# Kernel tuning notes

Measured on AMD Instinct MI355X. Metric: run time of the kernel, lower is better.

Reference implementation:

```python
import jax, jax.numpy as jnp
import numpy as np

VOCAB = 30000
FEAT = 30000
HID = 1024
EMB = 1024
B, LQ, LKV = 32, 256, 256


def setup_inputs() -> dict:
    key = jax.random.key(0)
    ks = jax.random.split(key, 8)
    captions = jax.random.randint(ks[0], (B, LKV), 0, VOCAB)
    targets_feature = jax.random.randint(ks[1], (B, LKV), 0, FEAT)
    hidden_state = jax.random.normal(ks[2], (B, LQ, HID), dtype=jnp.float32)
    feature_mask = jax.random.uniform(ks[3], (B, LQ, LKV), dtype=jnp.float32)
    # embeddings initialized uniform(-0.1, 0.1) per init_weights
    Wa = jax.random.uniform(ks[4], (VOCAB, HID), minval=-0.1, maxval=0.1, dtype=jnp.float32)
    Wc = jax.random.uniform(ks[5], (FEAT, HID), minval=-0.1, maxval=0.1, dtype=jnp.float32)
    r = np.sqrt(6.0) / np.sqrt(2 * HID + EMB)
    fc_w = jax.random.uniform(ks[6], (EMB, 2 * HID), minval=-r, maxval=r, dtype=jnp.float32)
    fc_b = jnp.zeros((EMB,), dtype=jnp.float32)
    return {"captions": captions, "hidden_state": hidden_state,
            "targets_feature": targets_feature, "feature_mask": feature_mask,
            "Wa": Wa, "Wc": Wc, "fc_w": fc_w, "fc_b": fc_b}


def reference(captions, hidden_state, targets_feature, feature_mask, Wa, Wc, fc_w, fc_b):
    ea = Wa[captions]           # [B, LKV, H]
    ec = Wc[targets_feature]    # [B, LKV, H]
    # u = hidden_state @ embedding_a^T : [B, LQ, LKV]
    u = jnp.einsum('bqh,bkh->bqk', hidden_state, ea)
    mask = jnp.clip(feature_mask, 0.0, 1.0)
    delta = jnp.exp(u) * mask
    p = delta / (jnp.sum(delta, axis=2, keepdims=True) + 1e-10)  # masked softmax-like weights
    # weighted value sum without materializing [B,LQ,LKV,H] broadcasts
    o = jnp.einsum('bqk,bkh->bqh', p, ec)
    o = jnp.concatenate([hidden_state, o], axis=2)               # [B, LQ, 2H]
    o = o @ fc_w.T + fc_b                                        # [B, LQ, EMB]
    o = o + 1e-10
    norm = jnp.sqrt(jnp.sum(o * o, axis=-1, keepdims=True)) + 1e-8
    return o / norm
```

## Files before the change

### kernel.cpp

```cpp
#include <hip/hip_runtime.h>
#include <hip/hip_bf16.h>

typedef __attribute__((ext_vector_type(8))) short short8;
typedef __attribute__((ext_vector_type(4))) float f32x4;
using bf16 = __hip_bfloat16;


__device__ __forceinline__ void glds16(const void* g, void* lds) {
  __builtin_amdgcn_global_load_lds(
      (const __attribute__((address_space(1))) void*)g,
      (__attribute__((address_space(3))) void*)lds, 16, 0, 0);
}

__global__ __launch_bounds__(256) void k1_prep(
    const int* __restrict__ captions, const float* __restrict__ Wa,
    const float* __restrict__ H, const float* __restrict__ fcw,
    const int* __restrict__ targets, const float* __restrict__ Wc,
    bf16* __restrict__ EA, bf16* __restrict__ X, bf16* __restrict__ FW,
    bf16* __restrict__ ECT) {
  __shared__ float T[64][67];
  int task = blockIdx.x;
  int tid = threadIdx.x;
  if (task < 17408) {
    const float* src;
    bf16* dst;
    int n;
    if (task < 8192) {
      src = Wa + (size_t)captions[task] * 1024;
      dst = EA + (size_t)task * 1024;
      n = 1024;
    } else if (task < 16384) {
      int t = task - 8192;
      src = H + (size_t)t * 1024;
      dst = X + (size_t)t * 2048;
      n = 1024;
    } else {
      int t = task - 16384;
      src = fcw + (size_t)t * 2048;
      dst = FW + (size_t)t * 2048;
      n = 2048;
    }
    for (int c = tid * 4; c < n; c += 1024) {
      float4 v = *(const float4*)(src + c);
      __hip_bfloat162 p0, p1;
      p0.x = __float2bfloat16(v.x); p0.y = __float2bfloat16(v.y);
      p1.x = __float2bfloat16(v.z); p1.y = __float2bfloat16(v.w);
      *(__hip_bfloat162*)(dst + c) = p0;
      *(__hip_bfloat162*)(dst + c + 2) = p1;
    }
    return;
  }
  int bid = task - 17408;
  int b = bid >> 6;
  int kt = (bid >> 4) & 3;
  int ht = bid & 15;
#pragma unroll
  for (int p = 0; p < 4; ++p) {
    int k = p * 16 + (tid >> 4);
    int idx = targets[b * 256 + kt * 64 + k];
    const float* s = Wc + (size_t)idx * 1024 + ht * 64 + (tid & 15) * 4;
    float4 v = *(const float4*)s;
    int c = (tid & 15) * 4;
    T[k][c] = v.x; T[k][c + 1] = v.y; T[k][c + 2] = v.z; T[k][c + 3] = v.w;
  }
  __syncthreads();
#pragma unroll
  for (int p = 0; p < 8; ++p) {
    int h = p * 8 + (tid >> 5);
    int k = (tid & 31) * 2;
    __hip_bfloat162 o;
    o.x = __float2bfloat16(T[k][h]);
    o.y = __float2bfloat16(T[k + 1][h]);
    *(__hip_bfloat162*)(ECT + ((size_t)b * 1024 + ht * 64 + h) * 256 + kt * 64 + k) = o;
  }
}

__global__ __launch_bounds__(256, 1) void k23_scores_pv(
    bf16* __restrict__ X, const bf16* __restrict__ EA,
    const bf16* __restrict__ ECT, const float* __restrict__ mask) {
  __shared__ __align__(16) char smem[16 * 1024 + 512 + 128 * 1024];
  bf16* p_lds = (bf16*)smem;
  float* red  = (float*)(smem + 16 * 1024);
  bf16* big   = (bf16*)(smem + 16 * 1024 + 512);

  int p = blockIdx.x;
  int wg = (p & 7) * 32 + (p >> 3);
  int b = wg >> 3;
  int mb = wg & 7;
  int tid = threadIdx.x, w = tid >> 6, l = tid & 63;

  const bf16* Ag = X + ((size_t)b * 256 + mb * 32) * 2048;
  const bf16* Bg = EA + (size_t)b * 256 * 1024;
  bf16* As = big;
  bf16* Bs = big + 32 * 64;

  f32x4 sacc[2][4];
  f32x4 zero = {0.f, 0.f, 0.f, 0.f};
#pragma unroll
  for (int m2 = 0; m2 < 2; ++m2)
#pragma unroll
    for (int n = 0; n < 4; ++n) sacc[m2][n] = zero;

  for (int kt = 0; kt < 16; ++kt) {
    {
      int row = tid >> 3, ss = (tid & 7) ^ (row & 7);
      glds16(Ag + (size_t)row * 2048 + kt * 64 + ss * 8,
             As + (size_t)w * 64 * 8);
    }
#pragma unroll
    for (int i = 0; i < 8; ++i) {
      int c = i * 256 + tid;
      int row = c >> 3, ss = (c & 7) ^ (row & 7);
      glds16(Bg + (size_t)row * 1024 + kt * 64 + ss * 8,
             Bs + (size_t)(i * 256 + w * 64) * 8);
    }
    __syncthreads();
#pragma unroll
    for (int kk = 0; kk < 2; ++kk) {
      short8 a2[2];
#pragma unroll
      for (int m2 = 0; m2 < 2; ++m2) {
        int ar = m2 * 16 + (l & 15);
        int sl = kk * 4 + (l >> 4);
        a2[m2] = *(const short8*)(As + ar * 64 + ((sl ^ (ar & 7)) * 8));
      }
#pragma unroll
      for (int n = 0; n < 4; ++n) {
        int rb = w * 64 + n * 16 + (l & 15);
        int sl = kk * 4 + (l >> 4);
        short8 bfr = *(const short8*)(Bs + rb * 64 + ((sl ^ (rb & 7)) * 8));
#pragma unroll
        for (int m2 = 0; m2 < 2; ++m2)
          sacc[m2][n] = __builtin_amdgcn_mfma_f32_16x16x32_bf16(
              a2[m2], bfr, sacc[m2][n], 0, 0, 0);
      }
    }
    __syncthreads();
  }

  const float* mrow = mask + ((size_t)b * 256 + mb * 32) * 256;
  float s[2][4] = {{0.f, 0.f, 0.f, 0.f}, {0.f, 0.f, 0.f, 0.f}};
#pragma unroll
  for (int m2 = 0; m2 < 2; ++m2)
#pragma unroll
    for (int n = 0; n < 4; ++n)
#pragma unroll
      for (int i = 0; i < 4; ++i) {
        int r = m2 * 16 + ((l >> 4) << 2) + i;
        int c = w * 64 + n * 16 + (l & 15);
        float mv = mrow[r * 256 + c];
        mv = fminf(fmaxf(mv, 0.f), 1.f);
        float ev = expf(sacc[m2][n][i]) * mv;
        sacc[m2][n][i] = ev;
        s[m2][i] += ev;
      }
#pragma unroll
  for (int msk = 1; msk < 16; msk <<= 1)
#pragma unroll
    for (int m2 = 0; m2 < 2; ++m2)
#pragma unroll
      for (int i = 0; i < 4; ++i) s[m2][i] += __shfl_xor(s[m2][i], msk, 64);
  if ((l & 15) == 0) {
#pragma unroll
    for (int m2 = 0; m2 < 2; ++m2)
#pragma unroll
      for (int i = 0; i < 4; ++i)
        red[w * 32 + m2 * 16 + ((l >> 4) << 2) + i] = s[m2][i];
  }
  __syncthreads();
  float inv[2][4];
#pragma unroll
  for (int m2 = 0; m2 < 2; ++m2)
#pragma unroll
    for (int i = 0; i < 4; ++i) {
      int r = m2 * 16 + ((l >> 4) << 2) + i;
      float tot = red[r] + red[32 + r] + red[64 + r] + red[96 + r];
      inv[m2][i] = 1.f / (tot + 1e-10f);
    }
#pragma unroll
  for (int m2 = 0; m2 < 2; ++m2)
#pragma unroll
    for (int n = 0; n < 4; ++n)
#pragma unroll
      for (int i = 0; i < 4; ++i) {
        int r = m2 * 16 + ((l >> 4) << 2) + i;
        int c = w * 64 + n * 16 + (l & 15);
        float pv = sacc[m2][n][i] * inv[m2][i];
        p_lds[r * 256 + (((c >> 3) ^ (r & 7)) << 3) + (c & 7)] =
            __float2bfloat16(pv);
      }
  __syncthreads();

  bf16* XO = X + ((size_t)b * 256 + mb * 32) * 2048 + 1024;
  for (int np = 0; np < 2; ++np) {
    f32x4 acc[2][8];
#pragma unroll
    for (int m2 = 0; m2 < 2; ++m2)
#pragma unroll
      for (int n = 0; n < 8; ++n) acc[m2][n] = zero;

#pragma unroll
    for (int it = 0; it < 16; ++it) {
      int g = it * 64 + l;
      int row = g >> 3, ss = (g & 7) ^ (row & 7);
      glds16(ECT + ((size_t)b * 1024 + np * 512 + w * 128 + row) * 256 + ss * 8,
             big + (size_t)(0 * 4 + w) * 8192 + (size_t)it * 512);
    }
    __syncthreads();
    for (int kt = 0; kt < 4; ++kt) {
      int cur = kt & 1;
      if (kt < 3) {
#pragma unroll
        for (int it = 0; it < 16; ++it) {
          int g = it * 64 + l;
          int row = g >> 3, ss = (g & 7) ^ (row & 7);
          glds16(ECT + ((size_t)b * 1024 + np * 512 + w * 128 + row) * 256 +
                     (kt + 1) * 64 + ss * 8,
                 big + (size_t)((cur ^ 1) * 4 + w) * 8192 + (size_t)it * 512);
        }
      }
      const bf16* Bw = big + (size_t)(cur * 4 + w) * 8192;
#pragma unroll
      for (int kk = 0; kk < 2; ++kk) {
        short8 a2[2];
#pragma unroll
        for (int m2 = 0; m2 < 2; ++m2) {
          int ar = m2 * 16 + (l & 15);
          int sl = kt * 8 + kk * 4 + (l >> 4);
          a2[m2] = *(const short8*)(p_lds + ar * 256 + ((sl ^ (ar & 7)) * 8));
        }
#pragma unroll
        for (int n = 0; n < 8; ++n) {
          int rb = n * 16 + (l & 15);
          int sl = kk * 4 + (l >> 4);
          short8 bfr = *(const short8*)(Bw + rb * 64 + ((sl ^ (rb & 7)) * 8));
#pragma unroll
          for (int m2 = 0; m2 < 2; ++m2)
            acc[m2][n] = __builtin_amdgcn_mfma_f32_16x16x32_bf16(
                a2[m2], bfr, acc[m2][n], 0, 0, 0);
        }
      }
      __syncthreads();
    }
#pragma unroll
    for (int m2 = 0; m2 < 2; ++m2)
#pragma unroll
      for (int n = 0; n < 8; ++n) {
        int rl = m2 * 16 + ((l >> 4) << 2);
        int col = np * 512 + w * 128 + n * 16 + (l & 15);
#pragma unroll
        for (int i = 0; i < 4; ++i)
          XO[(size_t)(rl + i) * 2048 + col] = __float2bfloat16(acc[m2][n][i]);
      }
  }
}

#define K4A (256 * 64)
#define K4B (128 * 64)

__device__ __forceinline__ void k4_stage(const bf16* __restrict__ Ag,
                                         const bf16* __restrict__ Bg, int kt,
                                         bf16* As, bf16* Bs, int tid, int w) {
#pragma unroll
  for (int i = 0; i < 4; ++i) {
    int c = i * 512 + tid;
    int row = c >> 3, ss = (c & 7) ^ (row & 7);
    glds16(Ag + (size_t)row * 2048 + kt * 64 + ss * 8,
           As + (size_t)(i * 512 + w * 64) * 8);
  }
#pragma unroll
  for (int i = 0; i < 2; ++i) {
    int c = i * 512 + tid;
    int row = c >> 3, ss = (c & 7) ^ (row & 7);
    glds16(Bg + (size_t)row * 2048 + kt * 64 + ss * 8,
           Bs + (size_t)(i * 512 + w * 64) * 8);
  }
}

__device__ __forceinline__ void k4_tile(const bf16* As, const bf16* Bs,
                                        int wr, int wc, int l,
                                        f32x4 (&acc)[4][4]) {
  short8 a[2][4], b[2][4];
#pragma unroll
  for (int kk = 0; kk < 2; ++kk)
#pragma unroll
    for (int n = 0; n < 4; ++n) {
      int row = wc * 64 + n * 16 + (l & 15);
      int slot = kk * 4 + (l >> 4);
      b[kk][n] = *(const short8*)(Bs + row * 64 + ((slot ^ (row & 7)) * 8));
    }
#pragma unroll
  for (int kk = 0; kk < 2; ++kk)
#pragma unroll
    for (int m = 0; m < 4; ++m) {
      int row = wr * 64 + m * 16 + (l & 15);
      int slot = kk * 4 + (l >> 4);
      a[kk][m] = *(const short8*)(As + row * 64 + ((slot ^ (row & 7)) * 8));
    }
  __builtin_amdgcn_s_setprio(1);
#pragma unroll
  for (int kk = 0; kk < 2; ++kk)
#pragma unroll
    for (int m = 0; m < 4; ++m)
#pragma unroll
      for (int n = 0; n < 4; ++n)
        acc[m][n] = __builtin_amdgcn_mfma_f32_16x16x32_bf16(
            a[kk][m], b[kk][n], acc[m][n], 0, 0, 0);
  __builtin_amdgcn_s_setprio(0);
}

__global__ __launch_bounds__(512, 1) void k4_fc(
    const bf16* __restrict__ X, const bf16* __restrict__ FW,
    const float* __restrict__ fcb, float* __restrict__ out) {
  __shared__ __align__(16) bf16 As[2][K4A];
  __shared__ __align__(16) bf16 Bs[2][K4B];
  int p = blockIdx.x;
  int wg = (p & 7) * 32 + (p >> 3);
  int mb = wg >> 3;
  int nb = wg & 7;
  int tid = threadIdx.x, w = tid >> 6, l = tid & 63;
  int wr = w >> 1, wc = w & 1;
  f32x4 acc[4][4];
  f32x4 zero = {0.f, 0.f, 0.f, 0.f};
#pragma unroll
  for (int m = 0; m < 4; ++m)
#pragma unroll
    for (int n = 0; n < 4; ++n) acc[m][n] = zero;

  const bf16* Ag = X + (size_t)mb * 256 * 2048;
  const bf16* Bg = FW + (size_t)nb * 128 * 2048;

  k4_stage(Ag, Bg, 0, As[0], Bs[0], tid, w);
  __syncthreads();
  for (int t = 0; t < 32; ++t) {
    int cur = t & 1;
    if (t < 31)
      k4_stage(Ag, Bg, t + 1, As[cur ^ 1], Bs[cur ^ 1], tid, w);
    k4_tile(As[cur], Bs[cur], wr, wc, l, acc);
    __syncthreads();
  }

  float bias[4];
#pragma unroll
  for (int n = 0; n < 4; ++n)
    bias[n] = fcb[nb * 128 + wc * 64 + n * 16 + (l & 15)];
#pragma unroll
  for (int m = 0; m < 4; ++m) {
    int rbase = mb * 256 + wr * 64 + m * 16 + ((l >> 4) << 2);
#pragma unroll
    for (int n = 0; n < 4; ++n) {
      int col = nb * 128 + wc * 64 + n * 16 + (l & 15);
#pragma unroll
      for (int i = 0; i < 4; ++i)
        out[(size_t)(rbase + i) * 1024 + col] = acc[m][n][i] + bias[n] + 1e-10f;
    }
  }
}

__global__ __launch_bounds__(256) void k5_norm(float* __restrict__ y) {
  __shared__ float red[4];
  int row = blockIdx.x;
  float* p = y + (size_t)row * 1024;
  int tid = threadIdx.x;
  float4 v = *(const float4*)(p + tid * 4);
  float ss = v.x * v.x + v.y * v.y + v.z * v.z + v.w * v.w;
#pragma unroll
  for (int m = 1; m < 64; m <<= 1) ss += __shfl_xor(ss, m, 64);
  if ((tid & 63) == 0) red[tid >> 6] = ss;
  __syncthreads();
  float tot = red[0] + red[1] + red[2] + red[3];
  float inv = 1.f / (sqrtf(tot) + 1e-8f);
  float4 o;
  o.x = v.x * inv; o.y = v.y * inv; o.z = v.z * inv; o.w = v.w * inv;
  *(float4*)(p + tid * 4) = o;
}

extern "C" void kernel_launch(void* const* d_in, const int* in_sizes, int n_in,
                              void* d_out, int out_size, void* d_ws, size_t ws_size,
                              hipStream_t stream) {
  const int* captions = (const int*)d_in[0];
  const float* H = (const float*)d_in[1];
  const int* targets = (const int*)d_in[2];
  const float* mask = (const float*)d_in[3];
  const float* Wa = (const float*)d_in[4];
  const float* Wc = (const float*)d_in[5];
  const float* fcw = (const float*)d_in[6];
  const float* fcb = (const float*)d_in[7];
  float* out = (float*)d_out;

  char* ws = (char*)d_ws;
  bf16* EA = (bf16*)(ws);
  bf16* ECT = (bf16*)(ws + (16u << 20));
  bf16* X = (bf16*)(ws + (36u << 20));
  bf16* FW = (bf16*)(ws + (68u << 20));

  k1_prep<<<19456, 256, 0, stream>>>(captions, Wa, H, fcw, targets, Wc,
                                     EA, X, FW, ECT);
  k23_scores_pv<<<256, 256, 0, stream>>>(X, EA, ECT, mask);
  k4_fc<<<256, 512, 0, stream>>>(X, FW, fcb, out);
  k5_norm<<<8192, 256, 0, stream>>>(out);
}
```

Baseline: 118.6 us.

## Fuse row L2 normalization into FC GEMM epilogue via grid-wide barrier

```diff
diff --git a/kernel.cpp b/kernel.cpp
--- a/kernel.cpp
+++ b/kernel.cpp
@@ -309,9 +309,10 @@
   __builtin_amdgcn_s_setprio(0);
 }
 
-__global__ __launch_bounds__(512, 1) void k4_fc(
+__global__ __launch_bounds__(512, 1) void k4_fc_norm(
     const bf16* __restrict__ X, const bf16* __restrict__ FW,
-    const float* __restrict__ fcb, float* __restrict__ out) {
+    const float* __restrict__ fcb, float* __restrict__ out,
+    float* __restrict__ ssqp, unsigned* __restrict__ cnt) {
   __shared__ __align__(16) bf16 As[2][K4A];
   __shared__ __align__(16) bf16 Bs[2][K4B];
   int p = blockIdx.x;
@@ -344,35 +345,62 @@
 #pragma unroll
   for (int n = 0; n < 4; ++n)
     bias[n] = fcb[nb * 128 + wc * 64 + n * 16 + (l & 15)];
+
+  float* ssq_lds = (float*)&As[0][0];
+  if (tid < 256) ssq_lds[tid] = 0.f;
+  __syncthreads();
+#pragma unroll
+  for (int m = 0; m < 4; ++m)
+#pragma unroll
+    for (int i = 0; i < 4; ++i) {
+      float rs = 0.f;
+#pragma unroll
+      for (int n = 0; n < 4; ++n) {
+        float v = acc[m][n][i] + bias[n] + 1e-10f;
+        acc[m][n][i] = v;
+        rs += v * v;
+      }
+      rs += __shfl_xor(rs, 1, 64);
+      rs += __shfl_xor(rs, 2, 64);
+      rs += __shfl_xor(rs, 4, 64);
+      rs += __shfl_xor(rs, 8, 64);
+      if ((l & 15) == 0)
+        atomicAdd(&ssq_lds[wr * 64 + m * 16 + ((l >> 4) << 2) + i], rs);
+    }
+  __syncthreads();
+  if (tid < 256)
+    ssqp[(size_t)nb * 8192 + mb * 256 + tid] = ssq_lds[tid];
+  __syncthreads();
+  if (tid == 0) {
+    __threadfence();
+    atomicAdd(cnt, 1u);
+    while (__hip_atomic_load(cnt, __ATOMIC_ACQUIRE,
+                             __HIP_MEMORY_SCOPE_AGENT) < 256u)
+      __builtin_amdgcn_s_sleep(2);
+  }
+  __syncthreads();
+  if (tid < 256) {
+    int r = mb * 256 + tid;
+    float ssum = 0.f;
+#pragma unroll
+    for (int j = 0; j < 8; ++j)
+      ssum += __hip_atomic_load(&ssqp[(size_t)j * 8192 + r], __ATOMIC_RELAXED,
+                                __HIP_MEMORY_SCOPE_AGENT);
+    ssq_lds[tid] = 1.f / (sqrtf(ssum) + 1e-8f);
+  }
+  __syncthreads();
 #pragma unroll
   for (int m = 0; m < 4; ++m) {
-    int rbase = mb * 256 + wr * 64 + m * 16 + ((l >> 4) << 2);
+    int rl = wr * 64 + m * 16 + ((l >> 4) << 2);
+    int rbase = mb * 256 + rl;
 #pragma unroll
     for (int n = 0; n < 4; ++n) {
       int col = nb * 128 + wc * 64 + n * 16 + (l & 15);
 #pragma unroll
       for (int i = 0; i < 4; ++i)
-        out[(size_t)(rbase + i) * 1024 + col] = acc[m][n][i] + bias[n] + 1e-10f;
-    }
-  }
-}
-
-__global__ __launch_bounds__(256) void k5_norm(float* __restrict__ y) {
-  __shared__ float red[4];
-  int row = blockIdx.x;
-  float* p = y + (size_t)row * 1024;
-  int tid = threadIdx.x;
-  float4 v = *(const float4*)(p + tid * 4);
-  float ss = v.x * v.x + v.y * v.y + v.z * v.z + v.w * v.w;
-#pragma unroll
-  for (int m = 1; m < 64; m <<= 1) ss += __shfl_xor(ss, m, 64);
-  if ((tid & 63) == 0) red[tid >> 6] = ss;
-  __syncthreads();
-  float tot = red[0] + red[1] + red[2] + red[3];
-  float inv = 1.f / (sqrtf(tot) + 1e-8f);
-  float4 o;
-  o.x = v.x * inv; o.y = v.y * inv; o.z = v.z * inv; o.w = v.w * inv;
-  *(float4*)(p + tid * 4) = o;
+        out[(size_t)(rbase + i) * 1024 + col] = acc[m][n][i] * ssq_lds[rl + i];
+    }
+  }
 }
 
 extern "C" void kernel_launch(void* const* d_in, const int* in_sizes, int n_in,
@@ -391,12 +419,14 @@
   char* ws = (char*)d_ws;
   bf16* EA = (bf16*)(ws);
   bf16* ECT = (bf16*)(ws + (16u << 20));
+  float* ssqp = (float*)(ws + (32u << 20));
+  unsigned* cnt = (unsigned*)(ws + (33u << 20));
   bf16* X = (bf16*)(ws + (36u << 20));
   bf16* FW = (bf16*)(ws + (68u << 20));
 
+  hipMemsetAsync(cnt, 0, 4, stream);
   k1_prep<<<19456, 256, 0, stream>>>(captions, Wa, H, fcw, targets, Wc,
                                      EA, X, FW, ECT);
   k23_scores_pv<<<256, 256, 0, stream>>>(X, EA, ECT, mask);
-  k4_fc<<<256, 512, 0, stream>>>(X, FW, fcb, out);
-  k5_norm<<<8192, 256, 0, stream>>>(out);
-}
+  k4_fc_norm<<<256, 512, 0, stream>>>(X, FW, fcb, out, ssqp, cnt);
+}
```

Measured after the change: 127.0 us. 1.07x slower.
